# Kernel tuning notes

Measured on AMD Instinct MI355X. Metric: run time of the kernel, lower is better.

## Reference

```python
import jax, jax.numpy as jnp
import numpy as np

B, SQ, SK, D = 8, 512, 512, 32


def _spd_cov(key, b, s, d):
    # random SPD covariance: A A^T + I
    a = 0.1 * jax.random.normal(key, (b, s, d, d), dtype=jnp.float32)
    return jnp.einsum('bsde,bsfe->bsdf', a, a) + jnp.eye(d, dtype=jnp.float32)


def setup_inputs() -> dict:
    key = jax.random.key(0)
    ks = jax.random.split(key, 6)
    return {
        'q_mean': jax.random.normal(ks[0], (B, SQ, D), dtype=jnp.float32),
        'q_cov': _spd_cov(ks[1], B, SQ, D),
        'k_mean': jax.random.normal(ks[2], (B, SK, D), dtype=jnp.float32),
        'k_cov': _spd_cov(ks[3], B, SK, D),
        'v_mean': jax.random.normal(ks[4], (B, SK, D), dtype=jnp.float32),
        'v_cov': _spd_cov(ks[5], B, SK, D),
    }


def reference(q_mean, q_cov, k_mean, k_cov, v_mean, v_cov):
    # Pairwise symmetric Gaussian JSD attention.
    # JSD = 0.5*(KL(p_q||p_k)+KL(p_k||p_q)); the log-det terms cancel:
    # JSD = 0.25*( tr(Sk^-1 Sq) + tr(Sq^-1 Sk) - 2D
    #              + dm^T (Sk^-1 + Sq^-1) dm ),  dm = mu_q - mu_k
    d = q_mean.shape[-1]
    q_inv = jnp.linalg.inv(q_cov)            # [B,Sq,D,D]
    k_inv = jnp.linalg.inv(k_cov)            # [B,Sk,D,D]
    tr_kq = jnp.einsum('bkde,bqed->bqk', k_inv, q_cov)
    tr_qk = jnp.einsum('bqde,bked->bqk', q_inv, k_cov)
    dm = q_mean[:, :, None, :] - k_mean[:, None, :, :]   # [B,Sq,Sk,D]
    quad = (jnp.einsum('bqkd,bkde,bqke->bqk', dm, k_inv, dm)
            + jnp.einsum('bqkd,bqde,bqke->bqk', dm, q_inv, dm))
    js = 0.25 * (tr_kq + tr_qk - 2.0 * d + quad)         # [B,Sq,Sk]
    score = jax.nn.softmax(js, axis=-1)
    out_mean = jnp.einsum('bqk,bkd->bqd', score, v_mean)
    out_cov = jnp.einsum('bqk,bkde->bqde', score, v_cov)
    return out_mean, out_cov
```

## Files before the change

kernel.cpp:

```cpp
#include <hip/hip_runtime.h>

#define NBATCH 8
#define SQL 512
#define SKL 512
#define DD 32
#define KF 1152
#define UT 528
#define NOUT 1056
#define NVT 1088
#define LDA 40

typedef short short8 __attribute__((ext_vector_type(8)));
typedef float f32x4 __attribute__((ext_vector_type(4)));
typedef unsigned short ushort_t;

__device__ __forceinline__ ushort_t f2bf(float f) {
    unsigned int u = __float_as_uint(f);
    return (ushort_t)((u + 0x7fffu + ((u >> 16) & 1u)) >> 16);
}
__device__ __forceinline__ float bf2f(ushort_t h) {
    return __uint_as_float(((unsigned int)h) << 16);
}
__device__ __forceinline__ void wsplit(ushort_t* __restrict__ h, ushort_t* __restrict__ l,
                                       size_t idx, float v) {
    ushort_t hb = f2bf(v);
    h[idx] = hb;
    l[idx] = f2bf(v - bf2f(hb));
}
__device__ __forceinline__ float rdlane(float x, int l) {
    return __int_as_float(__builtin_amdgcn_readlane(__float_as_int(x), l));
}

__global__ __launch_bounds__(64) void feat_kernel(
    const float* __restrict__ qm, const float* __restrict__ qc,
    const float* __restrict__ km, const float* __restrict__ kc,
    ushort_t* __restrict__ fqh, ushort_t* __restrict__ fql,
    ushort_t* __restrict__ fkh, ushort_t* __restrict__ fkl)
{
    const int qside = (blockIdx.y == 0);
    const float* mean = qside ? qm : km;
    const float* cov  = qside ? qc : kc;
    ushort_t* fh = qside ? fqh : fkh;
    ushort_t* fl = qside ? fql : fkl;

    const int site = blockIdx.x;
    const float* covp = cov + (size_t)site * (DD * DD);
    const float* mup  = mean + (size_t)site * DD;
    const size_t fo = (size_t)site * KF;
    const int lane = threadIdx.x;

    __shared__ float cov_s[DD][DD + 1];
    __shared__ float inv_s[DD][DD + 1];
    __shared__ float mu_s[DD];
    __shared__ float iv_s[DD];

    if (lane < DD) mu_s[lane] = mup[lane];

    float a[DD];
    if (lane < DD) {
        #pragma unroll
        for (int r = 0; r < DD; ++r) {
            float v = covp[r * DD + lane];
            a[r] = v;
            cov_s[r][lane] = v;
        }
    } else {
        const int c = lane - DD;
        #pragma unroll
        for (int r = 0; r < DD; ++r) a[r] = (r == c) ? 1.0f : 0.0f;
    }

    #pragma unroll
    for (int p = 0; p < DD; ++p) {
        float piv = rdlane(a[p], p);
        float rinv = 1.0f / piv;
        float t = a[p] * rinv;
        #pragma unroll
        for (int r = 0; r < DD; ++r) {
            if (r != p) {
                float fr = rdlane(a[r], p);
                a[r] = fmaf(-fr, t, a[r]);
            }
        }
        a[p] = t;
    }

    if (lane >= DD) {
        const int c = lane - DD;
        #pragma unroll
        for (int r = 0; r < DD; ++r) inv_s[r][c] = a[r];
    }
    __syncthreads();

    if (lane < DD) {
        float s = 0.f;
        #pragma unroll
        for (int e = 0; e < DD; ++e) s += inv_s[lane][e] * mu_s[e];
        iv_s[lane] = s;
    }
    __syncthreads();

    float bias = 0.f;
    #pragma unroll
    for (int d2 = 0; d2 < DD; ++d2) bias += mu_s[d2] * iv_s[d2];

    for (int idx = lane; idx < UT; idx += 64) {
        int d = (int)((65.0f - sqrtf(4225.0f - 8.0f * (float)idx)) * 0.5f);
        if (d > 0 && (d * (65 - d)) / 2 > idx) --d;
        if (((d + 1) * (64 - d)) / 2 <= idx) ++d;
        int off = (d * (65 - d)) / 2;
        int e = d + (idx - off);
        float Mv = cov_s[d][e] + mu_s[d] * mu_s[e];
        float Iv = 0.5f * (inv_s[d][e] + inv_s[e][d]);
        float w = (d == e) ? 1.0f : 2.0f;
        if (qside) { wsplit(fh, fl, fo + idx, w * Mv); wsplit(fh, fl, fo + UT + idx, w * Iv); }
        else       { wsplit(fh, fl, fo + idx, Iv);     wsplit(fh, fl, fo + UT + idx, Mv); }
    }
    if (lane < DD) {
        float ivv = iv_s[lane], muv = mu_s[lane];
        if (qside) { wsplit(fh, fl, fo + 2*UT + lane, -2.f * ivv); wsplit(fh, fl, fo + 2*UT + DD + lane, muv); }
        else       { wsplit(fh, fl, fo + 2*UT + lane, muv);        wsplit(fh, fl, fo + 2*UT + DD + lane, -2.f * ivv); }
    }
    if (lane == 32) wsplit(fh, fl, fo + 2*UT + 2*DD, qside ? 1.0f : bias);
    for (int i = 2*UT + 2*DD + 1 + lane; i < KF; i += 64) { fh[fo + i] = 0; fl[fo + i] = 0; }
}

template<int KSTRIDE, int KITERS, int MODE>
__global__ __launch_bounds__(256) void gemm_split(
    const ushort_t* __restrict__ Ah_g, const ushort_t* __restrict__ Al_g,
    const ushort_t* __restrict__ Bh_g, const ushort_t* __restrict__ Bl_g,
    float* __restrict__ C0, float* __restrict__ C1)
{
    const int b = blockIdx.z, mt = blockIdx.y, nt = blockIdx.x;
    const int tid = threadIdx.x, lane = tid & 63, wid = tid >> 6;
    const int wm = wid & 1, wn = wid >> 1;
    const int BROWS = MODE ? NVT : SKL;

    const ushort_t* Ah = Ah_g + ((size_t)b * SQL + mt * 128) * KSTRIDE;
    const ushort_t* Al = Al_g + ((size_t)b * SQL + mt * 128) * KSTRIDE;
    const ushort_t* Bh = Bh_g + ((size_t)b * BROWS + nt * 64) * KSTRIDE;
    const ushort_t* Bl = Bl_g + ((size_t)b * BROWS + nt * 64) * KSTRIDE;

    __shared__ __align__(16) ushort_t AsH[128 * LDA];
    __shared__ __align__(16) ushort_t AsL[128 * LDA];
    __shared__ __align__(16) ushort_t BsH[64 * LDA];
    __shared__ __align__(16) ushort_t BsL[64 * LDA];

    const int srow = tid >> 2;
    const int kp   = (tid & 3) * 8;

    const int fm = lane & 15;
    const int q8 = (lane >> 4) * 8;

    f32x4 acc[4][2];
    #pragma unroll
    for (int i = 0; i < 4; ++i)
        #pragma unroll
        for (int j = 0; j < 2; ++j)
            acc[i][j] = (f32x4){0.f, 0.f, 0.f, 0.f};

    for (int it = 0; it < KITERS; ++it) {
        const int k0 = it * 32;
        const uint4 a0 = *(const uint4*)(Ah + (size_t)srow        * KSTRIDE + k0 + kp);
        const uint4 a1 = *(const uint4*)(Ah + (size_t)(srow + 64) * KSTRIDE + k0 + kp);
        const uint4 a2 = *(const uint4*)(Al + (size_t)srow        * KSTRIDE + k0 + kp);
        const uint4 a3 = *(const uint4*)(Al + (size_t)(srow + 64) * KSTRIDE + k0 + kp);
        const uint4 b0 = *(const uint4*)(Bh + (size_t)srow        * KSTRIDE + k0 + kp);
        const uint4 b1 = *(const uint4*)(Bl + (size_t)srow        * KSTRIDE + k0 + kp);

        __syncthreads();
        *(uint4*)&AsH[srow        * LDA + kp] = a0;
        *(uint4*)&AsH[(srow + 64) * LDA + kp] = a1;
        *(uint4*)&AsL[srow        * LDA + kp] = a2;
        *(uint4*)&AsL[(srow + 64) * LDA + kp] = a3;
        *(uint4*)&BsH[srow        * LDA + kp] = b0;
        *(uint4*)&BsL[srow        * LDA + kp] = b1;
        __syncthreads();

        short8 ah[4], al[4], bh[2], bl[2];
        #pragma unroll
        for (int i = 0; i < 4; ++i) {
            const int r = wm * 64 + i * 16 + fm;
            ah[i] = *(const short8*)&AsH[r * LDA + q8];
            al[i] = *(const short8*)&AsL[r * LDA + q8];
        }
        #pragma unroll
        for (int j = 0; j < 2; ++j) {
            const int r = wn * 32 + j * 16 + fm;
            bh[j] = *(const short8*)&BsH[r * LDA + q8];
            bl[j] = *(const short8*)&BsL[r * LDA + q8];
        }
        #pragma unroll
        for (int i = 0; i < 4; ++i)
            #pragma unroll
            for (int j = 0; j < 2; ++j) {
                acc[i][j] = __builtin_amdgcn_mfma_f32_16x16x32_bf16(ah[i], bh[j], acc[i][j], 0, 0, 0);
                acc[i][j] = __builtin_amdgcn_mfma_f32_16x16x32_bf16(ah[i], bl[j], acc[i][j], 0, 0, 0);
                acc[i][j] = __builtin_amdgcn_mfma_f32_16x16x32_bf16(al[i], bh[j], acc[i][j], 0, 0, 0);
            }
    }

    const int crow0 = (lane >> 4) * 4;
    const int ccol = lane & 15;
    #pragma unroll
    for (int i = 0; i < 4; ++i) {
        const int m = mt * 128 + wm * 64 + i * 16 + crow0;
        #pragma unroll
        for (int j = 0; j < 2; ++j) {
            const int n = nt * 64 + wn * 32 + j * 16 + ccol;
            #pragma unroll
            for (int r = 0; r < 4; ++r) {
                const float v = acc[i][j][r];
                const size_t rowb = (size_t)b * SQL + (m + r);
                if (MODE == 0) {
                    C0[rowb * SKL + n] = 0.25f * v;
                } else {
                    if (n < DD)        C0[rowb * DD + n] = v;
                    else if (n < NOUT) C1[rowb * (DD * DD) + (n - DD)] = v;
                }
            }
        }
    }
}

__global__ __launch_bounds__(256) void softmax_rows(
    const float* __restrict__ js, ushort_t* __restrict__ ph, ushort_t* __restrict__ pl)
{
    const float* p = js + (size_t)blockIdx.x * SKL;
    const int tid = threadIdx.x;
    float2 v = *(const float2*)(p + 2 * tid);
    float m = fmaxf(v.x, v.y);
    #pragma unroll
    for (int o = 32; o > 0; o >>= 1) m = fmaxf(m, __shfl_xor(m, o));
    __shared__ float redm[4], reds[4];
    const int wid = tid >> 6, ln = tid & 63;
    if (ln == 0) redm[wid] = m;
    __syncthreads();
    m = fmaxf(fmaxf(redm[0], redm[1]), fmaxf(redm[2], redm[3]));
    float e0 = __expf(v.x - m), e1 = __expf(v.y - m);
    float s = e0 + e1;
    #pragma unroll
    for (int o = 32; o > 0; o >>= 1) s += __shfl_xor(s, o);
    if (ln == 0) reds[wid] = s;
    __syncthreads();
    s = reds[0] + reds[1] + reds[2] + reds[3];
    float rs = 1.0f / s;
    size_t o = (size_t)blockIdx.x * SKL + 2 * tid;
    wsplit(ph, pl, o,     e0 * rs);
    wsplit(ph, pl, o + 1, e1 * rs);
}

__global__ __launch_bounds__(256) void vsplit_kernel(
    const float* __restrict__ vmean, const float* __restrict__ vcov,
    ushort_t* __restrict__ vth, ushort_t* __restrict__ vtl)
{
    __shared__ float t[32][33];
    const int n0 = blockIdx.x * 32, k0 = blockIdx.y * 32, b = blockIdx.z;
    const int tx = threadIdx.x, ty = threadIdx.y;
    for (int r = ty; r < 32; r += 8) {
        const int k = k0 + r, n = n0 + tx;
        float v;
        if (n0 == 0)          v = vmean[((size_t)b * SKL + k) * DD + n];
        else if (n0 >= NOUT)  v = 0.f;
        else                  v = vcov[((size_t)b * SKL + k) * (DD * DD) + (n - DD)];
        t[tx][r] = v;
    }
    __syncthreads();
    for (int r = ty; r < 32; r += 8) {
        const int n = n0 + r, k = k0 + tx;
        const float v = t[r][tx];
        wsplit(vth, vtl, ((size_t)b * NVT + n) * SKL + k, v);
    }
}

extern "C" void kernel_launch(void* const* d_in, const int* in_sizes, int n_in,
                              void* d_out, int out_size, void* d_ws, size_t ws_size,
                              hipStream_t stream)
{
    const float* q_mean = (const float*)d_in[0];
    const float* q_cov  = (const float*)d_in[1];
    const float* k_mean = (const float*)d_in[2];
    const float* k_cov  = (const float*)d_in[3];
    const float* v_mean = (const float*)d_in[4];
    const float* v_cov  = (const float*)d_in[5];

    float* out_mean = (float*)d_out;
    float* out_cov  = out_mean + (size_t)NBATCH * SQL * DD;

    char* w = (char*)d_ws;
    const size_t FQN = (size_t)NBATCH * SQL * KF;
    ushort_t* fq_h = (ushort_t*)w;
    ushort_t* fq_l = fq_h + FQN;
    ushort_t* fk_h = fq_l + FQN;
    ushort_t* fk_l = fk_h + FQN;
    float*    js   = (float*)(fk_l + FQN);
    ushort_t* vt_h = fq_h;
    ushort_t* vt_l = fq_l;
    ushort_t* p_h  = fk_h;
    ushort_t* p_l  = fk_l;

    feat_kernel<<<dim3(NBATCH * SQL, 2), 64, 0, stream>>>(
        q_mean, q_cov, k_mean, k_cov, fq_h, fq_l, fk_h, fk_l);
    gemm_split<KF, KF / 32, 0><<<dim3(SKL / 64, SQL / 128, NBATCH), 256, 0, stream>>>(
        fq_h, fq_l, fk_h, fk_l, js, nullptr);
    vsplit_kernel<<<dim3(NVT / 32, SKL / 32, NBATCH), dim3(32, 8), 0, stream>>>(
        v_mean, v_cov, vt_h, vt_l);
    softmax_rows<<<NBATCH * SQL, 256, 0, stream>>>(js, p_h, p_l);
    gemm_split<SKL, SKL / 32, 1><<<dim3(NVT / 64, SQL / 128, NBATCH), 256, 0, stream>>>(
        p_h, p_l, vt_h, vt_l, out_mean, out_cov);
}
```

Before: 227.9 us.

## Pack four sites per feature block, use direct global-to-LDS loads, drop P low split

The feature kernel now handles four sites per 256-thread block with per-wave shared buffers and reads covariance directly from global memory. The 0.25 score scale is folded into the q-side features. Both GEMMs stage tiles with global_load_lds into unpadded LDS instead of going through registers. The softmax output is written as a single bf16 value, so the second GEMM skips the low-part A loads and one of its three MFMAs. Dropping the low part of the probabilities lowers precision, and the unpadded LDS layout may cause bank conflicts.

```diff
diff --git a/kernel.cpp b/kernel.cpp
--- a/kernel.cpp
+++ b/kernel.cpp
@@ -8,7 +8,6 @@
 #define UT 528
 #define NOUT 1056
 #define NVT 1088
-#define LDA 40
 
 typedef short short8 __attribute__((ext_vector_type(8)));
 typedef float f32x4 __attribute__((ext_vector_type(4)));
@@ -30,40 +29,46 @@
 __device__ __forceinline__ float rdlane(float x, int l) {
     return __int_as_float(__builtin_amdgcn_readlane(__float_as_int(x), l));
 }
-
-__global__ __launch_bounds__(64) void feat_kernel(
+__device__ __forceinline__ void gl_lds16(const ushort_t* g, ushort_t* l) {
+    __builtin_amdgcn_global_load_lds(
+        (const __attribute__((address_space(1))) void*)g,
+        (__attribute__((address_space(3))) void*)l, 16, 0, 0);
+}
+
+__global__ __launch_bounds__(256, 8) void feat_kernel(
     const float* __restrict__ qm, const float* __restrict__ qc,
     const float* __restrict__ km, const float* __restrict__ kc,
     ushort_t* __restrict__ fqh, ushort_t* __restrict__ fql,
     ushort_t* __restrict__ fkh, ushort_t* __restrict__ fkl)
 {
-    const int qside = (blockIdx.y == 0);
+    const int wid = threadIdx.x >> 6;
+    const int lane = threadIdx.x & 63;
+    const int gsite = blockIdx.x * 4 + wid;
+    const int qside = gsite < NBATCH * SQL;
+    const int site = qside ? gsite : gsite - NBATCH * SQL;
+
     const float* mean = qside ? qm : km;
     const float* cov  = qside ? qc : kc;
     ushort_t* fh = qside ? fqh : fkh;
     ushort_t* fl = qside ? fql : fkl;
 
-    const int site = blockIdx.x;
     const float* covp = cov + (size_t)site * (DD * DD);
     const float* mup  = mean + (size_t)site * DD;
     const size_t fo = (size_t)site * KF;
-    const int lane = threadIdx.x;
-
-    __shared__ float cov_s[DD][DD + 1];
-    __shared__ float inv_s[DD][DD + 1];
-    __shared__ float mu_s[DD];
-    __shared__ float iv_s[DD];
+
+    __shared__ float inv_s4[4][DD][DD + 1];
+    __shared__ float mu_s4[4][DD];
+    __shared__ float iv_s4[4][DD];
+    float (*inv_s)[DD + 1] = inv_s4[wid];
+    float* mu_s = mu_s4[wid];
+    float* iv_s = iv_s4[wid];
 
     if (lane < DD) mu_s[lane] = mup[lane];
 
     float a[DD];
     if (lane < DD) {
         #pragma unroll
-        for (int r = 0; r < DD; ++r) {
-            float v = covp[r * DD + lane];
-            a[r] = v;
-            cov_s[r][lane] = v;
-        }
+        for (int r = 0; r < DD; ++r) a[r] = covp[r * DD + lane];
     } else {
         const int c = lane - DD;
         #pragma unroll
@@ -110,18 +115,18 @@
         if (((d + 1) * (64 - d)) / 2 <= idx) ++d;
         int off = (d * (65 - d)) / 2;
         int e = d + (idx - off);
-        float Mv = cov_s[d][e] + mu_s[d] * mu_s[e];
+        float Mv = covp[d * DD + e] + mu_s[d] * mu_s[e];
         float Iv = 0.5f * (inv_s[d][e] + inv_s[e][d]);
-        float w = (d == e) ? 1.0f : 2.0f;
+        float w = (d == e) ? 0.25f : 0.5f;
         if (qside) { wsplit(fh, fl, fo + idx, w * Mv); wsplit(fh, fl, fo + UT + idx, w * Iv); }
         else       { wsplit(fh, fl, fo + idx, Iv);     wsplit(fh, fl, fo + UT + idx, Mv); }
     }
     if (lane < DD) {
         float ivv = iv_s[lane], muv = mu_s[lane];
-        if (qside) { wsplit(fh, fl, fo + 2*UT + lane, -2.f * ivv); wsplit(fh, fl, fo + 2*UT + DD + lane, muv); }
-        else       { wsplit(fh, fl, fo + 2*UT + lane, muv);        wsplit(fh, fl, fo + 2*UT + DD + lane, -2.f * ivv); }
-    }
-    if (lane == 32) wsplit(fh, fl, fo + 2*UT + 2*DD, qside ? 1.0f : bias);
+        if (qside) { wsplit(fh, fl, fo + 2*UT + lane, -0.5f * ivv); wsplit(fh, fl, fo + 2*UT + DD + lane, 0.25f * muv); }
+        else       { wsplit(fh, fl, fo + 2*UT + lane, muv);         wsplit(fh, fl, fo + 2*UT + DD + lane, -2.f * ivv); }
+    }
+    if (lane == 32) wsplit(fh, fl, fo + 2*UT + 2*DD, qside ? 0.25f : bias);
     for (int i = 2*UT + 2*DD + 1 + lane; i < KF; i += 64) { fh[fo + i] = 0; fl[fo + i] = 0; }
 }
 
@@ -131,6 +136,7 @@
     const ushort_t* __restrict__ Bh_g, const ushort_t* __restrict__ Bl_g,
     float* __restrict__ C0, float* __restrict__ C1)
 {
+    constexpr bool ASPLIT = (MODE == 0);
     const int b = blockIdx.z, mt = blockIdx.y, nt = blockIdx.x;
     const int tid = threadIdx.x, lane = tid & 63, wid = tid >> 6;
     const int wm = wid & 1, wn = wid >> 1;
@@ -141,13 +147,14 @@
     const ushort_t* Bh = Bh_g + ((size_t)b * BROWS + nt * 64) * KSTRIDE;
     const ushort_t* Bl = Bl_g + ((size_t)b * BROWS + nt * 64) * KSTRIDE;
 
-    __shared__ __align__(16) ushort_t AsH[128 * LDA];
-    __shared__ __align__(16) ushort_t AsL[128 * LDA];
-    __shared__ __align__(16) ushort_t BsH[64 * LDA];
-    __shared__ __align__(16) ushort_t BsL[64 * LDA];
-
-    const int srow = tid >> 2;
-    const int kp   = (tid & 3) * 8;
+    __shared__ __align__(16) ushort_t AsH[128 * 32];
+    __shared__ __align__(16) ushort_t AsL[ASPLIT ? 128 * 32 : 8];
+    __shared__ __align__(16) ushort_t BsH[64 * 32];
+    __shared__ __align__(16) ushort_t BsL[64 * 32];
+
+    const int r4 = lane >> 2, kp = (lane & 3) * 8;
+    const int arow0 = wid * 16 + r4,        aoff0 = wid * 512 + lane * 8;
+    const int arow1 = (wid + 4) * 16 + r4,  aoff1 = (wid + 4) * 512 + lane * 8;
 
     const int fm = lane & 15;
     const int q8 = (lane >> 4) * 8;
@@ -161,34 +168,29 @@
 
     for (int it = 0; it < KITERS; ++it) {
         const int k0 = it * 32;
-        const uint4 a0 = *(const uint4*)(Ah + (size_t)srow        * KSTRIDE + k0 + kp);
-        const uint4 a1 = *(const uint4*)(Ah + (size_t)(srow + 64) * KSTRIDE + k0 + kp);
-        const uint4 a2 = *(const uint4*)(Al + (size_t)srow        * KSTRIDE + k0 + kp);
-        const uint4 a3 = *(const uint4*)(Al + (size_t)(srow + 64) * KSTRIDE + k0 + kp);
-        const uint4 b0 = *(const uint4*)(Bh + (size_t)srow        * KSTRIDE + k0 + kp);
-        const uint4 b1 = *(const uint4*)(Bl + (size_t)srow        * KSTRIDE + k0 + kp);
-
         __syncthreads();
-        *(uint4*)&AsH[srow        * LDA + kp] = a0;
-        *(uint4*)&AsH[(srow + 64) * LDA + kp] = a1;
-        *(uint4*)&AsL[srow        * LDA + kp] = a2;
-        *(uint4*)&AsL[(srow + 64) * LDA + kp] = a3;
-        *(uint4*)&BsH[srow        * LDA + kp] = b0;
-        *(uint4*)&BsL[srow        * LDA + kp] = b1;
+        gl_lds16(Ah + (size_t)arow0 * KSTRIDE + k0 + kp, &AsH[aoff0]);
+        gl_lds16(Ah + (size_t)arow1 * KSTRIDE + k0 + kp, &AsH[aoff1]);
+        if (ASPLIT) {
+            gl_lds16(Al + (size_t)arow0 * KSTRIDE + k0 + kp, &AsL[aoff0]);
+            gl_lds16(Al + (size_t)arow1 * KSTRIDE + k0 + kp, &AsL[aoff1]);
+        }
+        gl_lds16(Bh + (size_t)arow0 * KSTRIDE + k0 + kp, &BsH[aoff0]);
+        gl_lds16(Bl + (size_t)arow0 * KSTRIDE + k0 + kp, &BsL[aoff0]);
         __syncthreads();
 
         short8 ah[4], al[4], bh[2], bl[2];
         #pragma unroll
         for (int i = 0; i < 4; ++i) {
             const int r = wm * 64 + i * 16 + fm;
-            ah[i] = *(const short8*)&AsH[r * LDA + q8];
-            al[i] = *(const short8*)&AsL[r * LDA + q8];
+            ah[i] = *(const short8*)&AsH[r * 32 + q8];
+            if (ASPLIT) al[i] = *(const short8*)&AsL[r * 32 + q8];
         }
         #pragma unroll
         for (int j = 0; j < 2; ++j) {
             const int r = wn * 32 + j * 16 + fm;
-            bh[j] = *(const short8*)&BsH[r * LDA + q8];
-            bl[j] = *(const short8*)&BsL[r * LDA + q8];
+            bh[j] = *(const short8*)&BsH[r * 32 + q8];
+            bl[j] = *(const short8*)&BsL[r * 32 + q8];
         }
         #pragma unroll
         for (int i = 0; i < 4; ++i)
@@ -196,7 +198,8 @@
             for (int j = 0; j < 2; ++j) {
                 acc[i][j] = __builtin_amdgcn_mfma_f32_16x16x32_bf16(ah[i], bh[j], acc[i][j], 0, 0, 0);
                 acc[i][j] = __builtin_amdgcn_mfma_f32_16x16x32_bf16(ah[i], bl[j], acc[i][j], 0, 0, 0);
-                acc[i][j] = __builtin_amdgcn_mfma_f32_16x16x32_bf16(al[i], bh[j], acc[i][j], 0, 0, 0);
+                if (ASPLIT)
+                    acc[i][j] = __builtin_amdgcn_mfma_f32_16x16x32_bf16(al[i], bh[j], acc[i][j], 0, 0, 0);
             }
     }
 
@@ -213,7 +216,7 @@
                 const float v = acc[i][j][r];
                 const size_t rowb = (size_t)b * SQL + (m + r);
                 if (MODE == 0) {
-                    C0[rowb * SKL + n] = 0.25f * v;
+                    C0[rowb * SKL + n] = v;
                 } else {
                     if (n < DD)        C0[rowb * DD + n] = v;
                     else if (n < NOUT) C1[rowb * (DD * DD) + (n - DD)] = v;
@@ -224,7 +227,7 @@
 }
 
 __global__ __launch_bounds__(256) void softmax_rows(
-    const float* __restrict__ js, ushort_t* __restrict__ ph, ushort_t* __restrict__ pl)
+    const float* __restrict__ js, ushort_t* __restrict__ ph)
 {
     const float* p = js + (size_t)blockIdx.x * SKL;
     const int tid = threadIdx.x;
@@ -246,8 +249,8 @@
     s = reds[0] + reds[1] + reds[2] + reds[3];
     float rs = 1.0f / s;
     size_t o = (size_t)blockIdx.x * SKL + 2 * tid;
-    wsplit(ph, pl, o,     e0 * rs);
-    wsplit(ph, pl, o + 1, e1 * rs);
+    ph[o]     = f2bf(e0 * rs);
+    ph[o + 1] = f2bf(e1 * rs);
 }
 
 __global__ __launch_bounds__(256) void vsplit_kernel(
@@ -297,15 +300,14 @@
     ushort_t* vt_h = fq_h;
     ushort_t* vt_l = fq_l;
     ushort_t* p_h  = fk_h;
-    ushort_t* p_l  = fk_l;
-
-    feat_kernel<<<dim3(NBATCH * SQL, 2), 64, 0, stream>>>(
+
+    feat_kernel<<<dim3(2 * NBATCH * SQL / 4), 256, 0, stream>>>(
         q_mean, q_cov, k_mean, k_cov, fq_h, fq_l, fk_h, fk_l);
     gemm_split<KF, KF / 32, 0><<<dim3(SKL / 64, SQL / 128, NBATCH), 256, 0, stream>>>(
         fq_h, fq_l, fk_h, fk_l, js, nullptr);
     vsplit_kernel<<<dim3(NVT / 32, SKL / 32, NBATCH), dim3(32, 8), 0, stream>>>(
         v_mean, v_cov, vt_h, vt_l);
-    softmax_rows<<<NBATCH * SQL, 256, 0, stream>>>(js, p_h, p_l);
+    softmax_rows<<<NBATCH * SQL, 256, 0, stream>>>(js, p_h);
     gemm_split<SKL, SKL / 32, 1><<<dim3(NVT / 64, SQL / 128, NBATCH), 256, 0, stream>>>(
-        p_h, p_l, vt_h, vt_l, out_mean, out_cov);
-}
+        p_h, nullptr, vt_h, vt_l, out_mean, out_cov);
+}
```

Result: no change. 225.1 us (-1.2%).
